# Kernel optimization log

Hardware: AMD Instinct MI355X
Metric: run time of the kernel (lower is better)

The kernel has to match this reference:

```python
import jax, jax.numpy as jnp
import numpy as np

N_ARY = 2
H = 128
X_SIZE = 128
DEPTH = 18  # levels in complete binary tree; n = 2^DEPTH - 1 = 262143 nodes


def setup_inputs() -> dict:
    key = jax.random.key(0)
    k0, k1, k2, k3 = jax.random.split(key, 4)
    n = (N_ARY ** DEPTH - 1) // (N_ARY - 1)
    x = jax.random.normal(k0, (n, X_SIZE), jnp.float32)
    W_w = jax.random.normal(k1, (2 * H, X_SIZE), jnp.float32) * 0.05
    W_b = jnp.zeros((2 * H,), jnp.float32)
    U_f = jax.random.normal(k2, (H, N_ARY * H), jnp.float32) * 0.05
    U_hc = jax.random.normal(k3, (H, N_ARY * H), jnp.float32) * 0.05
    return {"x": x, "W_w": W_w, "W_b": W_b, "U_f": U_f, "U_hc": U_hc, "depth": DEPTH}


def reference(x, W_w, W_b, U_f, U_hc, depth):
    """Tree-structured single-forget-gate MGU on a complete N_ARY tree.

    Node i (level-order) has children N_ARY*i+1 .. N_ARY*i+N_ARY. Levels are
    processed bottom-up (leaves first), matching DGL topological prop_nodes.
    """
    n_ary, h_size = N_ARY, H
    n = x.shape[0]
    wx = x @ W_w.T + W_b                      # [n, 2h]
    w_hc_x = wx[:, :h_size]                   # candidate pre-activation part
    w_f_x = wx[:, h_size:]                    # forget-gate pre-activation part
    h = jnp.zeros((n, h_size), x.dtype)
    for lvl in range(depth - 1, -1, -1):
        start = (n_ary ** lvl - 1) // (n_ary - 1)
        size = n_ary ** lvl
        whc = w_hc_x[start:start + size]
        wf = w_f_x[start:start + size]
        if lvl == depth - 1:
            # leaves: mailbox empty -> f_in = 0, h_cat = 0, h_sum = 0
            f = jax.nn.sigmoid(wf)
            new_h = (1.0 - f) * jnp.tanh(whc)
        else:
            # children of [start, start+size) occupy the contiguous next-level block
            child_start = n_ary * start + 1
            h_child = h[child_start:child_start + size * n_ary]
            h_child = h_child.reshape(size, n_ary, h_size)
            h_cat = h_child.reshape(size, n_ary * h_size)
            f = jax.nn.sigmoid(h_cat @ U_f.T + wf)
            f_rep = jnp.tile(f, (1, n_ary))
            h_cand = jnp.tanh(whc + (f_rep * h_cat) @ U_hc.T)
            new_h = f * h_child.sum(axis=1) + (1.0 - f) * h_cand
        h = h.at[start:start + size].set(new_h)
    return h
```

## Files before the change

### kernel.cpp

```cpp
#include <hip/hip_runtime.h>
#include <cmath>

#define NT 256

#define NTOT   262143
#define NINT   131071
#define LEAF0  131071
#define NLEAF  131072

#define WHC_OFF  0
#define WF_OFF   (NINT * 128)
#define WWT_OFF  (2 * NINT * 128)
#define UFT_OFF  (WWT_OFF + 128 * 256)
#define UHCT_OFF (UFT_OFF + 256 * 128)
#define WS_FLOATS (UHCT_OFF + 256 * 128)
#define WS_BYTES  ((size_t)WS_FLOATS * 4)

__device__ __forceinline__ float sigmoid_(float v) {
    return 1.0f / (1.0f + expf(-v));
}


__global__ __launch_bounds__(NT) void transpose_weights(
    const float* __restrict__ Ww, const float* __restrict__ Uf,
    const float* __restrict__ Uhc, float* __restrict__ ws)
{
    int t = blockIdx.x * NT + threadIdx.x;
    if (t < 128 * 256) {
        int k = t >> 8, j = t & 255;
        ws[WWT_OFF + t] = Ww[j * 128 + k];
    } else if (t < 2 * 32768) {
        int u = t - 32768;
        int k = u >> 7, j = u & 127;
        ws[UFT_OFF + u] = Uf[j * 256 + k];
    } else if (t < 3 * 32768) {
        int u = t - 2 * 32768;
        int k = u >> 7, j = u & 127;
        ws[UHCT_OFF + u] = Uhc[j * 256 + k];
    }
}

#define A_NB 16
__global__ __launch_bounds__(NT) void wx_internal(
    const float* __restrict__ x, const float* __restrict__ ws_all,
    const float* __restrict__ Wb, float* __restrict__ ws)
{
    __shared__ float sX[A_NB * 128];
    const float* wwt = ws_all + WWT_OFF;
    const int tid = threadIdx.x;
    const int nbase = blockIdx.x * A_NB;
    const int nb = min(A_NB, NINT - nbase);

    const int jq = tid & 63;  const int j0 = jq << 2;
    const int iq = tid >> 6;  const int i0 = iq << 2;

    {
        const float4* xg = (const float4*)(x + (size_t)nbase * 128);
        float4* sX4 = (float4*)sX;
        for (int idx = tid; idx < nb * 32; idx += NT) sX4[idx] = xg[idx];
    }
    __syncthreads();

    float acc[4][4];
#pragma unroll
    for (int j = 0; j < 4; ++j)
#pragma unroll
        for (int i = 0; i < 4; ++i) acc[j][i] = 0.f;

    const float4* sX4 = (const float4*)sX;
    for (int k0 = 0; k0 < 128; k0 += 8) {
        float4 w[8];
#pragma unroll
        for (int u = 0; u < 8; ++u)
            w[u] = *(const float4*)&wwt[(k0 + u) * 256 + j0];
        float4 a[4][2];
#pragma unroll
        for (int i = 0; i < 4; ++i) {
            a[i][0] = sX4[(i0 + i) * 32 + (k0 >> 2)];
            a[i][1] = sX4[(i0 + i) * 32 + (k0 >> 2) + 1];
        }
#pragma unroll
        for (int u = 0; u < 8; ++u) {
            const float* wp = (const float*)&w[u];
#pragma unroll
            for (int i = 0; i < 4; ++i) {
                float av = ((const float*)&a[i][u >> 2])[u & 3];
#pragma unroll
                for (int j = 0; j < 4; ++j)
                    acc[j][i] = fmaf(wp[j], av, acc[j][i]);
            }
        }
    }

    float* dst = (j0 < 128) ? (ws + WHC_OFF) : (ws + WF_OFF);
    const int jo = j0 & 127;
#pragma unroll
    for (int i = 0; i < 4; ++i) {
        if (i0 + i < nb) {
            float4 o;
            float* op = (float*)&o;
#pragma unroll
            for (int j = 0; j < 4; ++j) op[j] = acc[j][i] + Wb[j0 + j];
            *(float4*)&dst[(size_t)(nbase + i0 + i) * 128 + jo] = o;
        }
    }
}

#define L_NB 32
__global__ __launch_bounds__(NT) void leaf_kernel(
    const float* __restrict__ x, const float* __restrict__ ws_all,
    const float* __restrict__ Wb, float* __restrict__ h)
{
    __shared__ float sX[L_NB * 128];
    const float* wwt = ws_all + WWT_OFF;
    const int tid = threadIdx.x;
    const int nbase = blockIdx.x * L_NB;
    const int g0 = LEAF0 + nbase;

    const int jq = tid & 31;  const int j0 = jq << 2;
    const int iq = tid >> 5;  const int i0 = iq << 2;

    {
        const float4* xg = (const float4*)(x + (size_t)g0 * 128);
        float4* sX4 = (float4*)sX;
        for (int idx = tid; idx < L_NB * 32; idx += NT) sX4[idx] = xg[idx];
    }
    __syncthreads();

    float ahc[4][4], af[4][4];
#pragma unroll
    for (int j = 0; j < 4; ++j)
#pragma unroll
        for (int i = 0; i < 4; ++i) { ahc[j][i] = 0.f; af[j][i] = 0.f; }

    const float4* sX4 = (const float4*)sX;
    for (int k0 = 0; k0 < 128; k0 += 8) {
        float4 w0[8], w1[8];
#pragma unroll
        for (int u = 0; u < 8; ++u) {
            w0[u] = *(const float4*)&wwt[(k0 + u) * 256 + j0];
            w1[u] = *(const float4*)&wwt[(k0 + u) * 256 + 128 + j0];
        }
        float4 a[4][2];
#pragma unroll
        for (int i = 0; i < 4; ++i) {
            a[i][0] = sX4[(i0 + i) * 32 + (k0 >> 2)];
            a[i][1] = sX4[(i0 + i) * 32 + (k0 >> 2) + 1];
        }
#pragma unroll
        for (int u = 0; u < 8; ++u) {
            const float* w0p = (const float*)&w0[u];
            const float* w1p = (const float*)&w1[u];
#pragma unroll
            for (int i = 0; i < 4; ++i) {
                float av = ((const float*)&a[i][u >> 2])[u & 3];
#pragma unroll
                for (int j = 0; j < 4; ++j) {
                    ahc[j][i] = fmaf(w0p[j], av, ahc[j][i]);
                    af[j][i]  = fmaf(w1p[j], av, af[j][i]);
                }
            }
        }
    }

#pragma unroll
    for (int i = 0; i < 4; ++i) {
        float4 o;
        float* op = (float*)&o;
#pragma unroll
        for (int j = 0; j < 4; ++j) {
            float f = sigmoid_(af[j][i] + Wb[128 + j0 + j]);
            op[j] = (1.0f - f) * tanhf(ahc[j][i] + Wb[j0 + j]);
        }
        *(float4*)&h[(size_t)(g0 + i0 + i) * 128 + j0] = o;
    }
}

#define B_NB 32
__global__ __launch_bounds__(NT) void level_kernel(
    const float* __restrict__ ws_all, float* __restrict__ h,
    int start, int size)
{
    __shared__ float sH[B_NB * 256];
    const float* uft  = ws_all + UFT_OFF;
    const float* uhct = ws_all + UHCT_OFF;
    const float* whcw = ws_all + WHC_OFF;
    const float* wfw  = ws_all + WF_OFF;

    const int tid = threadIdx.x;
    const int nbase = blockIdx.x * B_NB;
    const int s0 = start + nbase;
    const int nb = min(B_NB, size - nbase);

    const int jq = tid & 31;  const int j0 = jq << 2;
    const int iq = tid >> 5;  const int i0 = iq << 2;

    {
        const float4* hg = (const float4*)(h + ((size_t)2 * s0 + 1) * 128);
        float4* sH4 = (float4*)sH;
        for (int idx = tid; idx < nb * 64; idx += NT) sH4[idx] = hg[idx];
    }
    __syncthreads();

    const float4* sH4 = (const float4*)sH;

    float fv[4][4];
#pragma unroll
    for (int j = 0; j < 4; ++j)
#pragma unroll
        for (int i = 0; i < 4; ++i) fv[j][i] = 0.f;

    for (int k0 = 0; k0 < 256; k0 += 8) {
        float4 w[8];
#pragma unroll
        for (int u = 0; u < 8; ++u)
            w[u] = *(const float4*)&uft[(k0 + u) * 128 + j0];
        float4 a[4][2];
#pragma unroll
        for (int i = 0; i < 4; ++i) {
            a[i][0] = sH4[(i0 + i) * 64 + (k0 >> 2)];
            a[i][1] = sH4[(i0 + i) * 64 + (k0 >> 2) + 1];
        }
#pragma unroll
        for (int u = 0; u < 8; ++u) {
            const float* wp = (const float*)&w[u];
#pragma unroll
            for (int i = 0; i < 4; ++i) {
                float av = ((const float*)&a[i][u >> 2])[u & 3];
#pragma unroll
                for (int j = 0; j < 4; ++j)
                    fv[j][i] = fmaf(wp[j], av, fv[j][i]);
            }
        }
    }
#pragma unroll
    for (int i = 0; i < 4; ++i) {
        float4 wfv = *(const float4*)&wfw[(size_t)(s0 + i0 + i) * 128 + j0];
        const float* wfp = (const float*)&wfv;
#pragma unroll
        for (int j = 0; j < 4; ++j)
            fv[j][i] = sigmoid_(fv[j][i] + wfp[j]);
    }

    __syncthreads();

    float hs[4][4];
#pragma unroll
    for (int i = 0; i < 4; ++i) {
        float4* row = (float4*)&sH[(i0 + i) * 256];
        float4 c0 = row[jq];
        float4 c1 = row[32 + jq];
        hs[0][i] = c0.x + c1.x;
        hs[1][i] = c0.y + c1.y;
        hs[2][i] = c0.z + c1.z;
        hs[3][i] = c0.w + c1.w;
        c0.x *= fv[0][i]; c0.y *= fv[1][i]; c0.z *= fv[2][i]; c0.w *= fv[3][i];
        c1.x *= fv[0][i]; c1.y *= fv[1][i]; c1.z *= fv[2][i]; c1.w *= fv[3][i];
        row[jq] = c0;
        row[32 + jq] = c1;
    }
    __syncthreads();

    float cv[4][4];
#pragma unroll
    for (int j = 0; j < 4; ++j)
#pragma unroll
        for (int i = 0; i < 4; ++i) cv[j][i] = 0.f;

    for (int k0 = 0; k0 < 256; k0 += 8) {
        float4 w[8];
#pragma unroll
        for (int u = 0; u < 8; ++u)
            w[u] = *(const float4*)&uhct[(k0 + u) * 128 + j0];
        float4 a[4][2];
#pragma unroll
        for (int i = 0; i < 4; ++i) {
            a[i][0] = sH4[(i0 + i) * 64 + (k0 >> 2)];
            a[i][1] = sH4[(i0 + i) * 64 + (k0 >> 2) + 1];
        }
#pragma unroll
        for (int u = 0; u < 8; ++u) {
            const float* wp = (const float*)&w[u];
#pragma unroll
            for (int i = 0; i < 4; ++i) {
                float av = ((const float*)&a[i][u >> 2])[u & 3];
#pragma unroll
                for (int j = 0; j < 4; ++j)
                    cv[j][i] = fmaf(wp[j], av, cv[j][i]);
            }
        }
    }

#pragma unroll
    for (int i = 0; i < 4; ++i) {
        if (i0 + i < nb) {
            float4 whcv = *(const float4*)&whcw[(size_t)(s0 + i0 + i) * 128 + j0];
            const float* wp = (const float*)&whcv;
            float4 o;
            float* op = (float*)&o;
#pragma unroll
            for (int j = 0; j < 4; ++j) {
                float t = tanhf(cv[j][i] + wp[j]);
                op[j] = fv[j][i] * hs[j][i] + (1.0f - fv[j][i]) * t;
            }
            *(float4*)&h[(size_t)(s0 + i0 + i) * 128 + j0] = o;
        }
    }
}


__global__ __launch_bounds__(NT) void fb_leaf(
    const float* __restrict__ x, const float* __restrict__ Ww,
    const float* __restrict__ Wb, float* __restrict__ h, int start, int size)
{
    __shared__ float sA[32 * 128];
    __shared__ float sW[16 * 260];
    const int tid = threadIdx.x;
    const int nbase = blockIdx.x * 32;
    const int s0 = start + nbase;
    const int nb = min(32, size - nbase);
    const int jq = tid & 31, iq = tid >> 5;
    const int j0 = jq << 2, i0 = iq << 2;
    {
        const float4* xg = (const float4*)(x + (size_t)s0 * 128);
        float4* sA4 = (float4*)sA;
        for (int idx = tid; idx < nb * 32; idx += NT) sA4[idx] = xg[idx];
    }
    float whc[4][4], wf[4][4];
#pragma unroll
    for (int j = 0; j < 4; ++j)
#pragma unroll
        for (int i = 0; i < 4; ++i) { whc[j][i] = 0.f; wf[j][i] = 0.f; }
    for (int k0 = 0; k0 < 128; k0 += 16) {
        __syncthreads();
        const float4* Wg = (const float4*)Ww;
        for (int idx = tid; idx < 256 * 4; idx += NT) {
            int j2 = idx >> 2, kq = idx & 3;
            float4 v = Wg[j2 * 32 + (k0 >> 2) + kq];
            int kb = kq << 2;
            sW[(kb + 0) * 260 + j2] = v.x; sW[(kb + 1) * 260 + j2] = v.y;
            sW[(kb + 2) * 260 + j2] = v.z; sW[(kb + 3) * 260 + j2] = v.w;
        }
        __syncthreads();
#pragma unroll
        for (int kk = 0; kk < 16; kk += 4) {
            float4 a4[4];
#pragma unroll
            for (int i = 0; i < 4; ++i)
                a4[i] = ((const float4*)sA)[(i0 + i) * 32 + ((k0 + kk) >> 2)];
#pragma unroll
            for (int u = 0; u < 4; ++u) {
                int k = kk + u;
                float4 w0 = *((const float4*)&sW[k * 260 + j0]);
                float4 w1 = *((const float4*)&sW[k * 260 + 128 + j0]);
                const float* w0p = (const float*)&w0;
                const float* w1p = (const float*)&w1;
#pragma unroll
                for (int i = 0; i < 4; ++i) {
                    float av = ((const float*)&a4[i])[u];
#pragma unroll
                    for (int j = 0; j < 4; ++j) {
                        whc[j][i] = fmaf(w0p[j], av, whc[j][i]);
                        wf[j][i]  = fmaf(w1p[j], av, wf[j][i]);
                    }
                }
            }
        }
    }
#pragma unroll
    for (int i = 0; i < 4; ++i) {
        if (i0 + i < nb) {
            float4 o; float* op = (float*)&o;
#pragma unroll
            for (int j = 0; j < 4; ++j) {
                float f = sigmoid_(wf[j][i] + Wb[128 + j0 + j]);
                op[j] = (1.0f - f) * tanhf(whc[j][i] + Wb[j0 + j]);
            }
            *(float4*)&h[((size_t)(s0 + i0 + i)) * 128 + j0] = o;
        }
    }
}

__global__ __launch_bounds__(NT) void fb_internal(
    const float* __restrict__ x, const float* __restrict__ Ww,
    const float* __restrict__ Wb, const float* __restrict__ Uf,
    const float* __restrict__ Uhc, float* __restrict__ h, int start, int size)
{
    __shared__ float sA[32 * 256];
    __shared__ float sW[4224];
    const int tid = threadIdx.x;
    const int nbase = blockIdx.x * 32;
    const int s0 = start + nbase;
    const int nb = min(32, size - nbase);
    const int jq = tid & 31, iq = tid >> 5;
    const int j0 = jq << 2, i0 = iq << 2;
    {
        const float4* xg = (const float4*)(x + (size_t)s0 * 128);
        float4* sA4 = (float4*)sA;
        for (int idx = tid; idx < nb * 32; idx += NT) sA4[idx] = xg[idx];
    }
    float whc[4][4], wf[4][4];
#pragma unroll
    for (int j = 0; j < 4; ++j)
#pragma unroll
        for (int i = 0; i < 4; ++i) { whc[j][i] = 0.f; wf[j][i] = 0.f; }
    for (int k0 = 0; k0 < 128; k0 += 16) {
        __syncthreads();
        const float4* Wg = (const float4*)Ww;
        for (int idx = tid; idx < 256 * 4; idx += NT) {
            int j2 = idx >> 2, kq = idx & 3;
            float4 v = Wg[j2 * 32 + (k0 >> 2) + kq];
            int kb = kq << 2;
            sW[(kb + 0) * 260 + j2] = v.x; sW[(kb + 1) * 260 + j2] = v.y;
            sW[(kb + 2) * 260 + j2] = v.z; sW[(kb + 3) * 260 + j2] = v.w;
        }
        __syncthreads();
#pragma unroll
        for (int kk = 0; kk < 16; kk += 4) {
            float4 a4[4];
#pragma unroll
            for (int i = 0; i < 4; ++i)
                a4[i] = ((const float4*)sA)[(i0 + i) * 32 + ((k0 + kk) >> 2)];
#pragma unroll
            for (int u = 0; u < 4; ++u) {
                int k = kk + u;
                float4 w0 = *((const float4*)&sW[k * 260 + j0]);
                float4 w1 = *((const float4*)&sW[k * 260 + 128 + j0]);
                const float* w0p = (const float*)&w0;
                const float* w1p = (const float*)&w1;
#pragma unroll
                for (int i = 0; i < 4; ++i) {
                    float av = ((const float*)&a4[i])[u];
#pragma unroll
                    for (int j = 0; j < 4; ++j) {
                        whc[j][i] = fmaf(w0p[j], av, whc[j][i]);
                        wf[j][i]  = fmaf(w1p[j], av, wf[j][i]);
                    }
                }
            }
        }
    }
#pragma unroll
    for (int j = 0; j < 4; ++j) {
        float bhc = Wb[j0 + j], bf = Wb[128 + j0 + j];
#pragma unroll
        for (int i = 0; i < 4; ++i) { whc[j][i] += bhc; wf[j][i] += bf; }
    }
    __syncthreads();
    {
        const float4* hg = (const float4*)(h + ((size_t)2 * s0 + 1) * 128);
        float4* sA4 = (float4*)sA;
        for (int idx = tid; idx < nb * 64; idx += NT) sA4[idx] = hg[idx];
    }
    float fv[4][4];
#pragma unroll
    for (int j = 0; j < 4; ++j)
#pragma unroll
        for (int i = 0; i < 4; ++i) fv[j][i] = 0.f;
    for (int k0 = 0; k0 < 256; k0 += 32) {
        __syncthreads();
        const float4* Ug = (const float4*)Uf;
        for (int idx = tid; idx < 128 * 8; idx += NT) {
            int j2 = idx >> 3, kq = idx & 7;
            float4 v = Ug[j2 * 64 + (k0 >> 2) + kq];
            int kb = kq << 2;
            sW[(kb + 0) * 132 + j2] = v.x; sW[(kb + 1) * 132 + j2] = v.y;
            sW[(kb + 2) * 132 + j2] = v.z; sW[(kb + 3) * 132 + j2] = v.w;
        }
        __syncthreads();
#pragma unroll
        for (int kk = 0; kk < 32; kk += 4) {
            float4 a4[4];
#pragma unroll
            for (int i = 0; i < 4; ++i)
                a4[i] = ((const float4*)sA)[(i0 + i) * 64 + ((k0 + kk) >> 2)];
#pragma unroll
            for (int u = 0; u < 4; ++u) {
                int k = kk + u;
                float4 w = *((const float4*)&sW[k * 132 + j0]);
                const float* wp = (const float*)&w;
#pragma unroll
                for (int i = 0; i < 4; ++i) {
                    float av = ((const float*)&a4[i])[u];
#pragma unroll
                    for (int j = 0; j < 4; ++j)
                        fv[j][i] = fmaf(wp[j], av, fv[j][i]);
                }
            }
        }
    }
#pragma unroll
    for (int j = 0; j < 4; ++j)
#pragma unroll
        for (int i = 0; i < 4; ++i)
            fv[j][i] = sigmoid_(fv[j][i] + wf[j][i]);
    __syncthreads();
    float hs[4][4];
#pragma unroll
    for (int i = 0; i < 4; ++i) {
        float4* row = (float4*)&sA[(i0 + i) * 256];
        float4 c0 = row[jq], c1 = row[32 + jq];
        hs[0][i] = c0.x + c1.x; hs[1][i] = c0.y + c1.y;
        hs[2][i] = c0.z + c1.z; hs[3][i] = c0.w + c1.w;
        c0.x *= fv[0][i]; c0.y *= fv[1][i]; c0.z *= fv[2][i]; c0.w *= fv[3][i];
        c1.x *= fv[0][i]; c1.y *= fv[1][i]; c1.z *= fv[2][i]; c1.w *= fv[3][i];
        row[jq] = c0; row[32 + jq] = c1;
    }
    float cv[4][4];
#pragma unroll
    for (int j = 0; j < 4; ++j)
#pragma unroll
        for (int i = 0; i < 4; ++i) cv[j][i] = 0.f;
    for (int k0 = 0; k0 < 256; k0 += 32) {
        __syncthreads();
        const float4* Ug = (const float4*)Uhc;
        for (int idx = tid; idx < 128 * 8; idx += NT) {
            int j2 = idx >> 3, kq = idx & 7;
            float4 v = Ug[j2 * 64 + (k0 >> 2) + kq];
            int kb = kq << 2;
            sW[(kb + 0) * 132 + j2] = v.x; sW[(kb + 1) * 132 + j2] = v.y;
            sW[(kb + 2) * 132 + j2] = v.z; sW[(kb + 3) * 132 + j2] = v.w;
        }
        __syncthreads();
#pragma unroll
        for (int kk = 0; kk < 32; kk += 4) {
            float4 a4[4];
#pragma unroll
            for (int i = 0; i < 4; ++i)
                a4[i] = ((const float4*)sA)[(i0 + i) * 64 + ((k0 + kk) >> 2)];
#pragma unroll
            for (int u = 0; u < 4; ++u) {
                int k = kk + u;
                float4 w = *((const float4*)&sW[k * 132 + j0]);
                const float* wp = (const float*)&w;
#pragma unroll
                for (int i = 0; i < 4; ++i) {
                    float av = ((const float*)&a4[i])[u];
#pragma unroll
                    for (int j = 0; j < 4; ++j)
                        cv[j][i] = fmaf(wp[j], av, cv[j][i]);
                }
            }
        }
    }
#pragma unroll
    for (int i = 0; i < 4; ++i) {
        if (i0 + i < nb) {
            float4 o; float* op = (float*)&o;
#pragma unroll
            for (int j = 0; j < 4; ++j) {
                float t = tanhf(cv[j][i] + whc[j][i]);
                op[j] = fv[j][i] * hs[j][i] + (1.0f - fv[j][i]) * t;
            }
            *(float4*)&h[((size_t)(s0 + i0 + i)) * 128 + j0] = o;
        }
    }
}


extern "C" void kernel_launch(void* const* d_in, const int* in_sizes, int n_in,
                              void* d_out, int out_size, void* d_ws, size_t ws_size,
                              hipStream_t stream)
{
    (void)in_sizes; (void)n_in; (void)out_size;
    const float* x   = (const float*)d_in[0];
    const float* Ww  = (const float*)d_in[1];
    const float* Wb  = (const float*)d_in[2];
    const float* Uf  = (const float*)d_in[3];
    const float* Uhc = (const float*)d_in[4];
    float* h = (float*)d_out;
    const int depth = 18;

    if (ws_size >= WS_BYTES) {
        float* ws = (float*)d_ws;
        transpose_weights<<<(3 * 32768 + NT - 1) / NT, NT, 0, stream>>>(Ww, Uf, Uhc, ws);
        wx_internal<<<(NINT + A_NB - 1) / A_NB, NT, 0, stream>>>(x, ws, Wb, ws);
        leaf_kernel<<<NLEAF / L_NB, NT, 0, stream>>>(x, ws, Wb, h);
        for (int lvl = depth - 2; lvl >= 0; --lvl) {
            int start = (1 << lvl) - 1;
            int size  = 1 << lvl;
            int grid  = (size + B_NB - 1) / B_NB;
            level_kernel<<<grid, NT, 0, stream>>>(ws, h, start, size);
        }
    } else {
        {
            int lvl = depth - 1;
            int start = (1 << lvl) - 1, size = 1 << lvl;
            fb_leaf<<<(size + 31) / 32, NT, 0, stream>>>(x, Ww, Wb, h, start, size);
        }
        for (int lvl = depth - 2; lvl >= 0; --lvl) {
            int start = (1 << lvl) - 1, size = 1 << lvl;
            fb_internal<<<(size + 31) / 32, NT, 0, stream>>>(x, Ww, Wb, Uf, Uhc, h, start, size);
        }
    }
}
```

Baseline: 966.4 us.

## Merge wx and leaf kernels, enlarge register tiles, fuse top levels into one block

Merges the internal-node input projection and the leaf computation into a single GEMM kernel over all nodes. Leaf rows pair the candidate and forget halves with a cross-lane shuffle. The level kernel's per-thread tile grows from 4x4 to 8x4 outputs, with 64 nodes per block. The six smallest levels (64 nodes down to the root) run in one single-block tail kernel to remove launch overhead and underfilled grids. The larger tiles raise register pressure and may lower occupancy. The tail kernel computes serially on one block.

```diff
diff --git a/kernel.cpp b/kernel.cpp
--- a/kernel.cpp
+++ b/kernel.cpp
@@ -40,19 +40,19 @@
     }
 }
 
-#define A_NB 16
-__global__ __launch_bounds__(NT) void wx_internal(
+__global__ __launch_bounds__(NT) void wx_all(
     const float* __restrict__ x, const float* __restrict__ ws_all,
-    const float* __restrict__ Wb, float* __restrict__ ws)
+    const float* __restrict__ Wb, float* __restrict__ ws, float* __restrict__ h)
 {
-    __shared__ float sX[A_NB * 128];
+    __shared__ __align__(16) float sX[64 * 128];
     const float* wwt = ws_all + WWT_OFF;
     const int tid = threadIdx.x;
-    const int nbase = blockIdx.x * A_NB;
-    const int nb = min(A_NB, NINT - nbase);
-
-    const int jq = tid & 63;  const int j0 = jq << 2;
-    const int iq = tid >> 6;  const int i0 = iq << 2;
+    const int nbase = blockIdx.x * 64;
+    const int nb = min(64, NTOT - nbase);
+
+    const int lane = tid & 63;
+    const int j0 = lane << 2;
+    const int i0 = (tid >> 6) << 4;
 
     {
         const float4* xg = (const float4*)(x + (size_t)nbase * 128);
@@ -61,250 +61,281 @@
     }
     __syncthreads();
 
-    float acc[4][4];
-#pragma unroll
-    for (int j = 0; j < 4; ++j)
-#pragma unroll
-        for (int i = 0; i < 4; ++i) acc[j][i] = 0.f;
+    float acc[16][4];
+#pragma unroll
+    for (int i = 0; i < 16; ++i)
+#pragma unroll
+        for (int j = 0; j < 4; ++j) acc[i][j] = 0.f;
 
     const float4* sX4 = (const float4*)sX;
     for (int k0 = 0; k0 < 128; k0 += 8) {
         float4 w[8];
 #pragma unroll
         for (int u = 0; u < 8; ++u)
-            w[u] = *(const float4*)&wwt[(k0 + u) * 256 + j0];
-        float4 a[4][2];
-#pragma unroll
-        for (int i = 0; i < 4; ++i) {
-            a[i][0] = sX4[(i0 + i) * 32 + (k0 >> 2)];
-            a[i][1] = sX4[(i0 + i) * 32 + (k0 >> 2) + 1];
-        }
-#pragma unroll
-        for (int u = 0; u < 8; ++u) {
-            const float* wp = (const float*)&w[u];
-#pragma unroll
-            for (int i = 0; i < 4; ++i) {
-                float av = ((const float*)&a[i][u >> 2])[u & 3];
+            w[u] = *(const float4*)&wwt[(size_t)(k0 + u) * 256 + j0];
+#pragma unroll
+        for (int i = 0; i < 16; ++i) {
+            float4 a0 = sX4[(i0 + i) * 32 + (k0 >> 2)];
+            float4 a1 = sX4[(i0 + i) * 32 + (k0 >> 2) + 1];
+            const float* ap0 = (const float*)&a0;
+            const float* ap1 = (const float*)&a1;
+#pragma unroll
+            for (int u = 0; u < 8; ++u) {
+                float av = (u < 4) ? ap0[u] : ap1[u - 4];
+                const float* wp = (const float*)&w[u];
 #pragma unroll
                 for (int j = 0; j < 4; ++j)
-                    acc[j][i] = fmaf(wp[j], av, acc[j][i]);
-            }
-        }
-    }
-
-    float* dst = (j0 < 128) ? (ws + WHC_OFF) : (ws + WF_OFF);
-    const int jo = j0 & 127;
-#pragma unroll
-    for (int i = 0; i < 4; ++i) {
-        if (i0 + i < nb) {
-            float4 o;
-            float* op = (float*)&o;
-#pragma unroll
-            for (int j = 0; j < 4; ++j) op[j] = acc[j][i] + Wb[j0 + j];
-            *(float4*)&dst[(size_t)(nbase + i0 + i) * 128 + jo] = o;
-        }
-    }
-}
-
-#define L_NB 32
-__global__ __launch_bounds__(NT) void leaf_kernel(
-    const float* __restrict__ x, const float* __restrict__ ws_all,
-    const float* __restrict__ Wb, float* __restrict__ h)
+                    acc[i][j] = fmaf(wp[j], av, acc[i][j]);
+            }
+        }
+    }
+
+    float4 bj = *(const float4*)&Wb[j0];
+    const float* bp = (const float*)&bj;
+    float* whcw = ws + WHC_OFF;
+    float* wfw  = ws + WF_OFF;
+    const bool isF = (lane >= 32);
+
+#pragma unroll
+    for (int i = 0; i < 16; ++i) {
+        int node = nbase + i0 + i;
+        if (node >= NTOT) continue;
+        float4 o4;
+        float* o = (float*)&o4;
+#pragma unroll
+        for (int j = 0; j < 4; ++j) o[j] = acc[i][j] + bp[j];
+        if (node < NINT) {
+            float* dst = isF ? (wfw + (size_t)node * 128 + (j0 - 128))
+                             : (whcw + (size_t)node * 128 + j0);
+            *(float4*)dst = o4;
+        } else {
+            float p[4];
+#pragma unroll
+            for (int j = 0; j < 4; ++j) p[j] = __shfl_xor(o[j], 32, 64);
+            if (!isF) {
+                float4 r;
+                float* rp = (float*)&r;
+#pragma unroll
+                for (int j = 0; j < 4; ++j) {
+                    float f = sigmoid_(p[j]);
+                    rp[j] = (1.0f - f) * tanhf(o[j]);
+                }
+                *(float4*)&h[(size_t)node * 128 + j0] = r;
+            }
+        }
+    }
+}
+
+__global__ __launch_bounds__(NT) void level_kernel(
+    const float* __restrict__ ws_all, float* __restrict__ h, int start)
 {
-    __shared__ float sX[L_NB * 128];
-    const float* wwt = ws_all + WWT_OFF;
-    const int tid = threadIdx.x;
-    const int nbase = blockIdx.x * L_NB;
-    const int g0 = LEAF0 + nbase;
-
-    const int jq = tid & 31;  const int j0 = jq << 2;
-    const int iq = tid >> 5;  const int i0 = iq << 2;
-
-    {
-        const float4* xg = (const float4*)(x + (size_t)g0 * 128);
-        float4* sX4 = (float4*)sX;
-        for (int idx = tid; idx < L_NB * 32; idx += NT) sX4[idx] = xg[idx];
-    }
-    __syncthreads();
-
-    float ahc[4][4], af[4][4];
-#pragma unroll
-    for (int j = 0; j < 4; ++j)
-#pragma unroll
-        for (int i = 0; i < 4; ++i) { ahc[j][i] = 0.f; af[j][i] = 0.f; }
-
-    const float4* sX4 = (const float4*)sX;
-    for (int k0 = 0; k0 < 128; k0 += 8) {
-        float4 w0[8], w1[8];
-#pragma unroll
-        for (int u = 0; u < 8; ++u) {
-            w0[u] = *(const float4*)&wwt[(k0 + u) * 256 + j0];
-            w1[u] = *(const float4*)&wwt[(k0 + u) * 256 + 128 + j0];
-        }
-        float4 a[4][2];
-#pragma unroll
-        for (int i = 0; i < 4; ++i) {
-            a[i][0] = sX4[(i0 + i) * 32 + (k0 >> 2)];
-            a[i][1] = sX4[(i0 + i) * 32 + (k0 >> 2) + 1];
-        }
-#pragma unroll
-        for (int u = 0; u < 8; ++u) {
-            const float* w0p = (const float*)&w0[u];
-            const float* w1p = (const float*)&w1[u];
-#pragma unroll
-            for (int i = 0; i < 4; ++i) {
-                float av = ((const float*)&a[i][u >> 2])[u & 3];
-#pragma unroll
-                for (int j = 0; j < 4; ++j) {
-                    ahc[j][i] = fmaf(w0p[j], av, ahc[j][i]);
-                    af[j][i]  = fmaf(w1p[j], av, af[j][i]);
-                }
-            }
-        }
-    }
-
-#pragma unroll
-    for (int i = 0; i < 4; ++i) {
-        float4 o;
-        float* op = (float*)&o;
-#pragma unroll
-        for (int j = 0; j < 4; ++j) {
-            float f = sigmoid_(af[j][i] + Wb[128 + j0 + j]);
-            op[j] = (1.0f - f) * tanhf(ahc[j][i] + Wb[j0 + j]);
-        }
-        *(float4*)&h[(size_t)(g0 + i0 + i) * 128 + j0] = o;
-    }
-}
-
-#define B_NB 32
-__global__ __launch_bounds__(NT) void level_kernel(
-    const float* __restrict__ ws_all, float* __restrict__ h,
-    int start, int size)
-{
-    __shared__ float sH[B_NB * 256];
+    __shared__ __align__(16) float sH[64 * 256];
     const float* uft  = ws_all + UFT_OFF;
     const float* uhct = ws_all + UHCT_OFF;
     const float* whcw = ws_all + WHC_OFF;
     const float* wfw  = ws_all + WF_OFF;
 
     const int tid = threadIdx.x;
-    const int nbase = blockIdx.x * B_NB;
-    const int s0 = start + nbase;
-    const int nb = min(B_NB, size - nbase);
+    const int s0 = start + blockIdx.x * 64;
 
     const int jq = tid & 31;  const int j0 = jq << 2;
-    const int iq = tid >> 5;  const int i0 = iq << 2;
+    const int iq = tid >> 5;  const int i0 = iq << 3;
 
     {
         const float4* hg = (const float4*)(h + ((size_t)2 * s0 + 1) * 128);
         float4* sH4 = (float4*)sH;
-        for (int idx = tid; idx < nb * 64; idx += NT) sH4[idx] = hg[idx];
+        for (int idx = tid; idx < 64 * 64; idx += NT) sH4[idx] = hg[idx];
     }
     __syncthreads();
 
     const float4* sH4 = (const float4*)sH;
 
-    float fv[4][4];
-#pragma unroll
-    for (int j = 0; j < 4; ++j)
-#pragma unroll
-        for (int i = 0; i < 4; ++i) fv[j][i] = 0.f;
+    float fv[8][4];
+#pragma unroll
+    for (int i = 0; i < 8; ++i)
+#pragma unroll
+        for (int j = 0; j < 4; ++j) fv[i][j] = 0.f;
 
     for (int k0 = 0; k0 < 256; k0 += 8) {
         float4 w[8];
 #pragma unroll
         for (int u = 0; u < 8; ++u)
-            w[u] = *(const float4*)&uft[(k0 + u) * 128 + j0];
-        float4 a[4][2];
-#pragma unroll
-        for (int i = 0; i < 4; ++i) {
-            a[i][0] = sH4[(i0 + i) * 64 + (k0 >> 2)];
-            a[i][1] = sH4[(i0 + i) * 64 + (k0 >> 2) + 1];
-        }
-#pragma unroll
-        for (int u = 0; u < 8; ++u) {
-            const float* wp = (const float*)&w[u];
-#pragma unroll
-            for (int i = 0; i < 4; ++i) {
-                float av = ((const float*)&a[i][u >> 2])[u & 3];
+            w[u] = *(const float4*)&uft[(size_t)(k0 + u) * 128 + j0];
+#pragma unroll
+        for (int i = 0; i < 8; ++i) {
+            float4 a0 = sH4[(i0 + i) * 64 + (k0 >> 2)];
+            float4 a1 = sH4[(i0 + i) * 64 + (k0 >> 2) + 1];
+            const float* ap0 = (const float*)&a0;
+            const float* ap1 = (const float*)&a1;
+#pragma unroll
+            for (int u = 0; u < 8; ++u) {
+                float av = (u < 4) ? ap0[u] : ap1[u - 4];
+                const float* wp = (const float*)&w[u];
 #pragma unroll
                 for (int j = 0; j < 4; ++j)
-                    fv[j][i] = fmaf(wp[j], av, fv[j][i]);
-            }
-        }
-    }
-#pragma unroll
-    for (int i = 0; i < 4; ++i) {
+                    fv[i][j] = fmaf(wp[j], av, fv[i][j]);
+            }
+        }
+    }
+#pragma unroll
+    for (int i = 0; i < 8; ++i) {
         float4 wfv = *(const float4*)&wfw[(size_t)(s0 + i0 + i) * 128 + j0];
         const float* wfp = (const float*)&wfv;
 #pragma unroll
         for (int j = 0; j < 4; ++j)
-            fv[j][i] = sigmoid_(fv[j][i] + wfp[j]);
+            fv[i][j] = sigmoid_(fv[i][j] + wfp[j]);
     }
 
     __syncthreads();
 
-    float hs[4][4];
-#pragma unroll
-    for (int i = 0; i < 4; ++i) {
+    float hs[8][4];
+#pragma unroll
+    for (int i = 0; i < 8; ++i) {
         float4* row = (float4*)&sH[(i0 + i) * 256];
         float4 c0 = row[jq];
         float4 c1 = row[32 + jq];
-        hs[0][i] = c0.x + c1.x;
-        hs[1][i] = c0.y + c1.y;
-        hs[2][i] = c0.z + c1.z;
-        hs[3][i] = c0.w + c1.w;
-        c0.x *= fv[0][i]; c0.y *= fv[1][i]; c0.z *= fv[2][i]; c0.w *= fv[3][i];
-        c1.x *= fv[0][i]; c1.y *= fv[1][i]; c1.z *= fv[2][i]; c1.w *= fv[3][i];
+        hs[i][0] = c0.x + c1.x;
+        hs[i][1] = c0.y + c1.y;
+        hs[i][2] = c0.z + c1.z;
+        hs[i][3] = c0.w + c1.w;
+        c0.x *= fv[i][0]; c0.y *= fv[i][1]; c0.z *= fv[i][2]; c0.w *= fv[i][3];
+        c1.x *= fv[i][0]; c1.y *= fv[i][1]; c1.z *= fv[i][2]; c1.w *= fv[i][3];
         row[jq] = c0;
         row[32 + jq] = c1;
     }
     __syncthreads();
 
-    float cv[4][4];
-#pragma unroll
-    for (int j = 0; j < 4; ++j)
-#pragma unroll
-        for (int i = 0; i < 4; ++i) cv[j][i] = 0.f;
+    float cv[8][4];
+#pragma unroll
+    for (int i = 0; i < 8; ++i)
+#pragma unroll
+        for (int j = 0; j < 4; ++j) cv[i][j] = 0.f;
 
     for (int k0 = 0; k0 < 256; k0 += 8) {
         float4 w[8];
 #pragma unroll
         for (int u = 0; u < 8; ++u)
-            w[u] = *(const float4*)&uhct[(k0 + u) * 128 + j0];
-        float4 a[4][2];
-#pragma unroll
-        for (int i = 0; i < 4; ++i) {
-            a[i][0] = sH4[(i0 + i) * 64 + (k0 >> 2)];
-            a[i][1] = sH4[(i0 + i) * 64 + (k0 >> 2) + 1];
-        }
-#pragma unroll
-        for (int u = 0; u < 8; ++u) {
-            const float* wp = (const float*)&w[u];
-#pragma unroll
-            for (int i = 0; i < 4; ++i) {
-                float av = ((const float*)&a[i][u >> 2])[u & 3];
+            w[u] = *(const float4*)&uhct[(size_t)(k0 + u) * 128 + j0];
+#pragma unroll
+        for (int i = 0; i < 8; ++i) {
+            float4 a0 = sH4[(i0 + i) * 64 + (k0 >> 2)];
+            float4 a1 = sH4[(i0 + i) * 64 + (k0 >> 2) + 1];
+            const float* ap0 = (const float*)&a0;
+            const float* ap1 = (const float*)&a1;
+#pragma unroll
+            for (int u = 0; u < 8; ++u) {
+                float av = (u < 4) ? ap0[u] : ap1[u - 4];
+                const float* wp = (const float*)&w[u];
 #pragma unroll
                 for (int j = 0; j < 4; ++j)
-                    cv[j][i] = fmaf(wp[j], av, cv[j][i]);
-            }
-        }
-    }
-
-#pragma unroll
-    for (int i = 0; i < 4; ++i) {
-        if (i0 + i < nb) {
-            float4 whcv = *(const float4*)&whcw[(size_t)(s0 + i0 + i) * 128 + j0];
-            const float* wp = (const float*)&whcv;
-            float4 o;
-            float* op = (float*)&o;
-#pragma unroll
-            for (int j = 0; j < 4; ++j) {
-                float t = tanhf(cv[j][i] + wp[j]);
-                op[j] = fv[j][i] * hs[j][i] + (1.0f - fv[j][i]) * t;
-            }
-            *(float4*)&h[(size_t)(s0 + i0 + i) * 128 + j0] = o;
-        }
+                    cv[i][j] = fmaf(wp[j], av, cv[i][j]);
+            }
+        }
+    }
+
+#pragma unroll
+    for (int i = 0; i < 8; ++i) {
+        float4 whcv = *(const float4*)&whcw[(size_t)(s0 + i0 + i) * 128 + j0];
+        const float* wp = (const float*)&whcv;
+        float4 o;
+        float* op = (float*)&o;
+#pragma unroll
+        for (int j = 0; j < 4; ++j) {
+            float t = tanhf(cv[i][j] + wp[j]);
+            op[j] = fv[i][j] * hs[i][j] + (1.0f - fv[i][j]) * t;
+        }
+        *(float4*)&h[(size_t)(s0 + i0 + i) * 128 + j0] = o;
+    }
+}
+
+__global__ __launch_bounds__(NT) void tail_kernel(
+    const float* __restrict__ ws_all, float* __restrict__ h)
+{
+    __shared__ __align__(16) float bufA[64 * 128];
+    __shared__ __align__(16) float bufB[32 * 128];
+    __shared__ __align__(16) float sF[8 * 128];
+    const float* uft  = ws_all + UFT_OFF;
+    const float* uhct = ws_all + UHCT_OFF;
+    const float* whcw = ws_all + WHC_OFF;
+    const float* wfw  = ws_all + WF_OFF;
+
+    const int tid = threadIdx.x;
+    const int jq = tid & 31;  const int j0 = jq << 2;
+    const int iq = tid >> 5;
+
+    {
+        const float4* hg = (const float4*)(h + (size_t)63 * 128);
+        float4* b4 = (float4*)bufA;
+        for (int idx = tid; idx < 64 * 32; idx += NT) b4[idx] = hg[idx];
+    }
+    __syncthreads();
+
+    float* child = bufA;
+    float* cur   = bufB;
+
+    for (int lvl = 5; lvl >= 0; --lvl) {
+        const int start = (1 << lvl) - 1;
+        const int size  = 1 << lvl;
+        for (int pass = 0; pass < size; pass += 8) {
+            const int ni = pass + iq;
+            const bool act = (ni < size);
+            float f[4] = {0.f, 0.f, 0.f, 0.f};
+            if (act) {
+                const float* hc = child + ni * 256;
+                float fv[4] = {0.f, 0.f, 0.f, 0.f};
+                for (int k = 0; k < 256; k += 4) {
+#pragma unroll
+                    for (int u = 0; u < 4; ++u) {
+                        float av = hc[k + u];
+                        float4 w = *(const float4*)&uft[(size_t)(k + u) * 128 + j0];
+                        fv[0] = fmaf(w.x, av, fv[0]);
+                        fv[1] = fmaf(w.y, av, fv[1]);
+                        fv[2] = fmaf(w.z, av, fv[2]);
+                        fv[3] = fmaf(w.w, av, fv[3]);
+                    }
+                }
+                const int gn = start + ni;
+                float4 wfv = *(const float4*)&wfw[(size_t)gn * 128 + j0];
+                const float* wfp = (const float*)&wfv;
+#pragma unroll
+                for (int j = 0; j < 4; ++j) {
+                    f[j] = sigmoid_(fv[j] + wfp[j]);
+                    sF[iq * 128 + j0 + j] = f[j];
+                }
+            }
+            __syncthreads();
+            if (act) {
+                const float* hc = child + ni * 256;
+                const float* fr = sF + iq * 128;
+                float cv[4] = {0.f, 0.f, 0.f, 0.f};
+                for (int k = 0; k < 256; k += 4) {
+#pragma unroll
+                    for (int u = 0; u < 4; ++u) {
+                        float av = hc[k + u] * fr[(k + u) & 127];
+                        float4 w = *(const float4*)&uhct[(size_t)(k + u) * 128 + j0];
+                        cv[0] = fmaf(w.x, av, cv[0]);
+                        cv[1] = fmaf(w.y, av, cv[1]);
+                        cv[2] = fmaf(w.z, av, cv[2]);
+                        cv[3] = fmaf(w.w, av, cv[3]);
+                    }
+                }
+                const int gn = start + ni;
+                float4 whcv = *(const float4*)&whcw[(size_t)gn * 128 + j0];
+                const float* wp = (const float*)&whcv;
+                float4 o;
+                float* op = (float*)&o;
+#pragma unroll
+                for (int j = 0; j < 4; ++j) {
+                    float hsum = hc[j0 + j] + hc[128 + j0 + j];
+                    float t = tanhf(cv[j] + wp[j]);
+                    op[j] = f[j] * hsum + (1.0f - f[j]) * t;
+                }
+                *(float4*)&cur[ni * 128 + j0] = o;
+                *(float4*)&h[(size_t)gn * 128 + j0] = o;
+            }
+            __syncthreads();
+        }
+        float* t = child; child = cur; cur = t;
     }
 }
 
@@ -574,14 +605,13 @@
     if (ws_size >= WS_BYTES) {
         float* ws = (float*)d_ws;
         transpose_weights<<<(3 * 32768 + NT - 1) / NT, NT, 0, stream>>>(Ww, Uf, Uhc, ws);
-        wx_internal<<<(NINT + A_NB - 1) / A_NB, NT, 0, stream>>>(x, ws, Wb, ws);
-        leaf_kernel<<<NLEAF / L_NB, NT, 0, stream>>>(x, ws, Wb, h);
-        for (int lvl = depth - 2; lvl >= 0; --lvl) {
+        wx_all<<<(NTOT + 63) / 64, NT, 0, stream>>>(x, ws, Wb, ws, h);
+        for (int lvl = 16; lvl >= 6; --lvl) {
             int start = (1 << lvl) - 1;
             int size  = 1 << lvl;
-            int grid  = (size + B_NB - 1) / B_NB;
-            level_kernel<<<grid, NT, 0, stream>>>(ws, h, start, size);
-        }
+            level_kernel<<<size / 64, NT, 0, stream>>>(ws, h, start);
+        }
+        tail_kernel<<<1, NT, 0, stream>>>(ws, h);
     } else {
         {
             int lvl = depth - 1;
```

New measurement: 1.119 ms. 1.16x slower.
